# Performance work log

Hardware: AMD Instinct MI355X
Metric: run time of the kernel (lower is better)

## Reference

```python
import jax, jax.numpy as jnp
import numpy as np

DIM = 512
HEADS = 8
DIM_HEAD = 64
HIDDEN = HEADS * DIM_HEAD
SCALE = DIM_HEAD ** -0.5


def rmsnorm_ch(x, g):
    # F.normalize over channel dim (axis=1), then * g * sqrt(C)
    # x: [b, c, l], g: [c]
    n = jnp.maximum(jnp.linalg.norm(x, axis=1, keepdims=True), 1e-12)
    c = x.shape[1]
    return (x / n) * g[None, :, None] * (c ** 0.5)


def setup_inputs() -> dict:
    key = jax.random.key(0)
    ks = jax.random.split(key, 6)
    b, l = 8, 4096
    x = jax.random.normal(ks[0], (b, DIM, l), dtype=jnp.float32)
    g_in = jnp.ones((DIM,), dtype=jnp.float32)
    # conv1d kernel_size=1 == matmul; kaiming-ish init scale
    w_qkv = jax.random.normal(ks[1], (3 * HIDDEN, DIM), dtype=jnp.float32) * (1.0 / np.sqrt(DIM))
    w_out = jax.random.normal(ks[2], (DIM, HIDDEN), dtype=jnp.float32) * (1.0 / np.sqrt(HIDDEN))
    b_out = jax.random.normal(ks[3], (DIM,), dtype=jnp.float32) * 0.01
    g_out = jnp.ones((DIM,), dtype=jnp.float32)
    return {"x": x, "g_in": g_in, "w_qkv": w_qkv, "w_out": w_out, "b_out": b_out, "g_out": g_out}


def reference(x, g_in, w_qkv, w_out, b_out, g_out):
    b, c, l = x.shape
    residual = x
    xn = rmsnorm_ch(x, g_in)                       # [b, c, l]
    qkv = jnp.einsum('oc,bcl->bol', w_qkv, xn)     # [b, 3*hidden, l]
    q, k, v = jnp.split(qkv, 3, axis=1)            # each [b, hidden, l]
    def to_heads(t):
        return t.reshape(b, HEADS, DIM_HEAD, l)    # [b, h, d, l]
    q, k, v = to_heads(q), to_heads(k), to_heads(v)
    q = jax.nn.softmax(q, axis=2) * SCALE          # softmax over head-dim d
    k = jax.nn.softmax(k, axis=3)                  # softmax over sequence l
    context = jnp.einsum('bhdn,bhen->bhde', k, v)  # [b, h, d, e]
    out = jnp.einsum('bhde,bhdn->bhen', context, q)  # [b, h, e, l]
    out = out.reshape(b, HIDDEN, l)
    o = jnp.einsum('ch,bhl->bcl', w_out, out) + b_out[None, :, None]
    o = rmsnorm_ch(o, g_out)
    return o + residual
```

## Files before the change

kernel.cpp:

```cpp
#include <hip/hip_runtime.h>


#define BB 8
#define CC 512
#define LL 4096
#define HH 8
#define DH 64
#define TC 1536

__device__ __constant__ const float SQRT_C = 22.62741699796952f;
#define SCALE_Q 0.125f

typedef unsigned short bfr_t;
typedef __attribute__((ext_vector_type(8))) short short8;
typedef __attribute__((ext_vector_type(4))) float f32x4;

__device__ __forceinline__ float bf2f(bfr_t v) {
  union { unsigned u; float f; } c; c.u = ((unsigned)v) << 16; return c.f;
}
__device__ __forceinline__ bfr_t f2bf(float f) {
  union { float f; unsigned u; } c; c.f = f;
  unsigned u = c.u + 0x7fffu + ((c.u >> 16) & 1u);
  return (bfr_t)(u >> 16);
}

__device__ __forceinline__ void load_lds16(const bfr_t* g, short* l) {
  __builtin_amdgcn_global_load_lds(
      (const __attribute__((address_space(1))) void*)g,
      (__attribute__((address_space(3))) void*)l, 16, 0, 0);
}

__global__ __launch_bounds__(256) void conv_bf16_2(
    const float* __restrict__ in1, bfr_t* __restrict__ o1, int n1,
    const float* __restrict__ in2, bfr_t* __restrict__ o2, int n2) {
  int i8 = (blockIdx.x * 256 + threadIdx.x) * 8;
  const float* src;
  bfr_t* dst;
  if (i8 < n1) { src = in1 + i8; dst = o1 + i8; }
  else {
    int j8 = i8 - n1;
    if (j8 >= n2) return;
    src = in2 + j8; dst = o2 + j8;
  }
  f32x4 a = *(const f32x4*)src;
  f32x4 b = *(const f32x4*)(src + 4);
  union { short s[8]; f32x4 v; } pk;
#pragma unroll
  for (int u = 0; u < 4; ++u) { pk.s[u] = (short)f2bf(a[u]); pk.s[u + 4] = (short)f2bf(b[u]); }
  *(f32x4*)dst = pk.v;
}

__global__ __launch_bounds__(256) void fused_norm_transpose(
    const float* __restrict__ x, const float* __restrict__ g,
    bfr_t* __restrict__ xt) {
  __shared__ float tile[64][65];
  __shared__ float red[4][64];
  __shared__ float invn_s[64];
  int b = blockIdx.y, l0 = blockIdx.x * 64;
  int t = threadIdx.x, ll = t & 63, cg = t >> 6;
  const float* xb = x + (size_t)b * CC * LL + l0;
  float vals[8][16];
  float ss = 0.f;
#pragma unroll
  for (int ch = 0; ch < 8; ++ch) {
    int c0 = ch * 64;
#pragma unroll
    for (int i = 0; i < 16; ++i) {
      int c = i * 4 + cg;
      float v = xb[(size_t)(c0 + c) * LL + ll];
      vals[ch][i] = v;
      ss += v * v;
    }
  }
  red[cg][ll] = ss;
  __syncthreads();
  if (cg == 0) {
    float s = red[0][ll] + red[1][ll] + red[2][ll] + red[3][ll];
    invn_s[ll] = SQRT_C / fmaxf(sqrtf(s), 1e-12f);
  }
  __syncthreads();
  int lw = t >> 2, ccw = (t & 3) * 16;
  float iv = invn_s[lw];
#pragma unroll
  for (int ch = 0; ch < 8; ++ch) {
    int c0 = ch * 64;
#pragma unroll
    for (int i = 0; i < 16; ++i) tile[i * 4 + cg][ll] = vals[ch][i];
    __syncthreads();
    union { short s[16]; f32x4 v[2]; } pk;
#pragma unroll
    for (int u = 0; u < 16; ++u) {
      int c = ccw + u;
      pk.s[u] = (short)f2bf(tile[c][lw] * g[c0 + c] * iv);
    }
    bfr_t* dst = xt + ((size_t)b * LL + l0 + lw) * CC + c0 + ccw;
    *(f32x4*)dst = pk.v[0];
    *(f32x4*)(dst + 8) = pk.v[1];
    __syncthreads();
  }
}

#define NT 8

__device__ __forceinline__ void stage_half(const bfr_t* g, short* l, int wid) {
  load_lds16(g + (size_t)wid * 8192,        l + wid * 1024);
  load_lds16(g + (size_t)wid * 8192 + 4096, l + wid * 1024 + 512);
}

#define CFENCE asm volatile("" ::: "memory")
#define LGKM0 asm volatile("s_waitcnt lgkmcnt(0)" ::: "memory")
#define VMC0  asm volatile("s_waitcnt vmcnt(0)" ::: "memory")
#define SB    __builtin_amdgcn_sched_barrier(0)
#define BAR   do { CFENCE; __builtin_amdgcn_s_barrier(); CFENCE; } while (0)
#define PRIO1 __builtin_amdgcn_s_setprio(1)
#define PRIO0 __builtin_amdgcn_s_setprio(0)

#define DSR(dst, addr, LIT) \
  asm volatile("ds_read_b128 %0, %1 offset:" #LIT : "=v"(dst) : "v"(addr))

#define RD_A(S, L0, L1, L2, L3) do {           \
    DSR(S[0], aAs0, L0); DSR(S[1], aAs1, L0);  \
    DSR(S[2], aAs0, L1); DSR(S[3], aAs1, L1);  \
    DSR(S[4], aAs0, L2); DSR(S[5], aAs1, L2);  \
    DSR(S[6], aAs0, L3); DSR(S[7], aAs1, L3); } while (0)
#define RD_B(S, L0, L1) do {                   \
    DSR(S[0], bBs0, L0); DSR(S[1], bBs1, L0);  \
    DSR(S[2], bBs0, L1); DSR(S[3], bBs1, L1); } while (0)

#define MMA8(QM, QN, AS, BS) do {                                            \
    _Pragma("unroll") for (int i_ = 0; i_ < 4; ++i_)                         \
      _Pragma("unroll") for (int j_ = 0; j_ < 2; ++j_) {                     \
        acc[(QM)*4+i_][(QN)*2+j_] = __builtin_amdgcn_mfma_f32_16x16x32_bf16( \
            AS[i_*2+0], BS[j_*2+0], acc[(QM)*4+i_][(QN)*2+j_], 0, 0, 0);     \
        acc[(QM)*4+i_][(QN)*2+j_] = __builtin_amdgcn_mfma_f32_16x16x32_bf16( \
            AS[i_*2+1], BS[j_*2+1], acc[(QM)*4+i_][(QN)*2+j_], 0, 0, 0);     \
      }                                                                      \
  } while (0)

#define STAGE_T(J, D) do {                                                   \
    stage_half(pA0 + (J) * 64, As + (D) * 16384, wid);                       \
    stage_half(pA1 + (J) * 64, As + (D) * 16384 + 8192, wid);                \
    stage_half(pB0 + (J) * 64, Bs + (D) * 16384, wid);                       \
    stage_half(pB1 + (J) * 64, Bs + (D) * 16384 + 8192, wid);                \
  } while (0)

#define TILE_E(KT) do {                                                      \
                                      \
    PRIO1; RD_B(bS1, 4096, 6144); MMA8(0, 0, aS0, bS0); PRIO0; LGKM0; SB;    \
                                      \
    PRIO1; RD_A(aS1, 8192, 10240, 12288, 14336); MMA8(0, 1, aS0, bS1);       \
    PRIO0; LGKM0; SB;                                                        \
         \
    if ((KT) < 7) { VMC0; }                                                  \
    BAR;                                                                     \
    if ((KT) <= 5) STAGE_T((KT) + 2, 0);                                     \
    PRIO1;                                                                   \
    if ((KT) < 7) RD_A(aS0, 32768, 34816, 36864, 38912);                     \
    MMA8(1, 1, aS1, bS1); PRIO0; LGKM0; SB;                                  \
            \
    PRIO1; MMA8(1, 0, aS1, bS0); PRIO0;                                      \
    if ((KT) < 7) RD_B(bS0, 32768, 34816);                                   \
    LGKM0; SB;                                                               \
  } while (0)

#define TILE_O(KT) do {                                                      \
    PRIO1; RD_B(bS1, 36864, 38912); MMA8(0, 0, aS0, bS0); PRIO0; LGKM0; SB;  \
    PRIO1; RD_A(aS1, 40960, 43008, 45056, 47104); MMA8(0, 1, aS0, bS1);      \
    PRIO0; LGKM0; SB;                                                        \
    if ((KT) < 7) { VMC0; }                                                  \
    BAR;                                                                     \
    if ((KT) <= 5) STAGE_T((KT) + 2, 1);                                     \
    PRIO1;                                                                   \
    if ((KT) < 7) RD_A(aS0, 0, 2048, 4096, 6144);                            \
    MMA8(1, 1, aS1, bS1); PRIO0; LGKM0; SB;                                  \
    PRIO1; MMA8(1, 0, aS1, bS0); PRIO0;                                      \
    if ((KT) < 7) RD_B(bS0, 0, 2048);                                        \
    LGKM0; SB;                                                               \
  } while (0)

__global__ __launch_bounds__(512, 2) void gemm256(
    const bfr_t* __restrict__ A, const bfr_t* __restrict__ Bt,
    bfr_t* __restrict__ Cout, const float* __restrict__ bias, int M) {
  __shared__ short lds[65536];
  short* As = lds;
  short* Bs = lds + 32768;

  int nwg = gridDim.x;
  int gy = M >> 8;
  int bid = blockIdx.x;
  int logical = (bid & 7) * (nwg >> 3) + (bid >> 3);
  int perz = (LL / 256) * gy;
  int bz = logical / perz;
  int rem = logical - bz * perz;
  int bx = rem / gy;
  int by = rem - bx * gy;

  int m0 = by * 256, n0 = bx * 256;
  int t = threadIdx.x, lane = t & 63, wid = t >> 6;
  int quad = lane >> 4, r16 = lane & 15;
  int wm = wid >> 2, wn = wid & 3;
  int soff = (lane >> 3) * 512 + (((lane & 7) ^ (lane >> 3)) * 8);
  int slot0 = (quad ^ (lane & 7)) * 8;
  int slot1 = ((4 + quad) ^ (lane & 7)) * 8;

  unsigned lb = (unsigned)(uintptr_t)(__attribute__((address_space(3))) short*)lds;
  unsigned aAs0 = lb + (unsigned)(wm * 16384 + r16 * 128 + slot0 * 2);
  unsigned aAs1 = lb + (unsigned)(wm * 16384 + r16 * 128 + slot1 * 2);
  unsigned bbase = 65536u + (unsigned)((wn >> 1) * 16384 + ((wn & 1) * 64 + r16) * 128);
  unsigned bBs0 = lb + bbase + (unsigned)(slot0 * 2);
  unsigned bBs1 = lb + bbase + (unsigned)(slot1 * 2);

  const bfr_t* pA0 = A + (size_t)m0 * 512 + soff;
  const bfr_t* pA1 = pA0 + (size_t)128 * 512;
  const bfr_t* pB0 = Bt + (size_t)bz * LL * 512 + (size_t)n0 * 512 + soff;
  const bfr_t* pB1 = pB0 + (size_t)128 * 512;

  f32x4 acc[8][4] = {};
  short8 aS0[8], aS1[8];
  short8 bS0[4], bS1[4];

  STAGE_T(0, 0);
  STAGE_T(1, 1);
  asm volatile("s_waitcnt vmcnt(8)" ::: "memory");
  BAR;
  RD_A(aS0, 0, 2048, 4096, 6144);
  RD_B(bS0, 0, 2048);
  LGKM0; SB;

  TILE_E(0); TILE_O(1); TILE_E(2); TILE_O(3);
  TILE_E(4); TILE_O(5); TILE_E(6); TILE_O(7);

  bfr_t* Cb = Cout + (size_t)bz * M * LL;
  int crow = m0 + wm * 128 + quad * 4;
  int ccol = n0 + wn * 64 + r16;
#pragma unroll
  for (int am = 0; am < 8; ++am) {
    int rbase = crow + (am >> 2) * 64 + (am & 3) * 16;
#pragma unroll
    for (int reg = 0; reg < 4; ++reg) {
      int row = rbase + reg;
      float bi = bias ? bias[row] : 0.f;
#pragma unroll
      for (int an = 0; an < 4; ++an) {
        int col = ccol + (an >> 1) * 32 + (an & 1) * 16;
        Cb[(size_t)row * LL + col] = f2bf(acc[am][an][reg] + bi);
      }
    }
  }
}

__global__ __launch_bounds__(256) void context_mfma(
    const bfr_t* __restrict__ qkv, float* __restrict__ ctx_p,
    float* __restrict__ ksum_p) {
  __shared__ float red[4][4096];
  int s = blockIdx.x, bh = blockIdx.y;
  int b = bh >> 3, h = bh & 7;
  int t = threadIdx.x, lane = t & 63, wid = t >> 6;
  int quad = lane >> 4, r = lane & 15;
  const bfr_t* kb = qkv + ((size_t)b * TC + 512 + h * 64) * LL;
  const bfr_t* vb = qkv + ((size_t)b * TC + 1024 + h * 64) * LL;
  int n_base = s * 512 + wid * 128;
  f32x4 acc[4][4] = {};
  float ps[4] = {};
#pragma unroll
  for (int ks = 0; ks < 4; ++ks) {
    int n0 = n_base + ks * 32;
    short8 af[4], bf8[4];
#pragma unroll
    for (int i = 0; i < 4; ++i) {
      union { short s[8]; short8 v8; } uk;
      uk.v8 = *(const short8*)&kb[(size_t)(i * 16 + r) * LL + n0 + quad * 8];
#pragma unroll
      for (int jj = 0; jj < 8; ++jj) {
        float e = __expf(bf2f((bfr_t)uk.s[jj]));
        uk.s[jj] = (short)f2bf(e);
        ps[i] += e;
      }
      af[i] = uk.v8;
      bf8[i] = *(const short8*)&vb[(size_t)(i * 16 + r) * LL + n0 + quad * 8];
    }
#pragma unroll
    for (int i = 0; i < 4; ++i)
#pragma unroll
      for (int j = 0; j < 4; ++j)
        acc[i][j] = __builtin_amdgcn_mfma_f32_16x16x32_bf16(af[i], bf8[j],
                                                            acc[i][j], 0, 0, 0);
  }
#pragma unroll
  for (int i = 0; i < 4; ++i) {
    ps[i] += __shfl_xor(ps[i], 16, 64);
    ps[i] += __shfl_xor(ps[i], 32, 64);
  }
  if (quad == 0) {
#pragma unroll
    for (int i = 0; i < 4; ++i) red[wid][i * 16 + r] = ps[i];
  }
  __syncthreads();
  if (t < 64)
    ksum_p[((size_t)bh * 8 + s) * 64 + t] =
        red[0][t] + red[1][t] + red[2][t] + red[3][t];
  __syncthreads();
#pragma unroll
  for (int i = 0; i < 4; ++i)
#pragma unroll
    for (int j = 0; j < 4; ++j)
#pragma unroll
      for (int reg = 0; reg < 4; ++reg)
        red[wid][(i * 16 + quad * 4 + reg) * 64 + j * 16 + r] = acc[i][j][reg];
  __syncthreads();
  float* out = ctx_p + ((size_t)bh * 8 + s) * 4096;
#pragma unroll
  for (int u = 0; u < 16; ++u) {
    int idx = u * 256 + t;
    out[idx] = red[0][idx] + red[1][idx] + red[2][idx] + red[3][idx];
  }
}

__global__ __launch_bounds__(256) void context_reduce(
    const float* __restrict__ ctx_p, const float* __restrict__ ksum_p,
    bfr_t* __restrict__ ctx_bf) {
  __shared__ float zinv[64];
  int bh = blockIdx.x;
  int t = threadIdx.x;
  if (t < 64) {
    float s = 0.f;
#pragma unroll
    for (int s8 = 0; s8 < 8; ++s8) s += ksum_p[((size_t)bh * 8 + s8) * 64 + t];
    zinv[t] = 1.f / s;
  }
  __syncthreads();
#pragma unroll
  for (int i = 0; i < 16; ++i) {
    int idx = i * 256 + t;
    int d = idx >> 6;
    float sum = 0.f;
#pragma unroll
    for (int s = 0; s < 8; ++s) sum += ctx_p[((size_t)bh * 8 + s) * 4096 + idx];
    ctx_bf[(size_t)bh * 4096 + idx] = f2bf(sum * zinv[d]);
  }
}

__global__ __launch_bounds__(256) void apply_fused(
    const bfr_t* __restrict__ qkv, const bfr_t* __restrict__ ctx_bf,
    bfr_t* __restrict__ out_t) {
  int b = blockIdx.z, h = blockIdx.y;
  int t = threadIdx.x, lane = t & 63, wid = t >> 6;
  int quad = lane >> 4, r = lane & 15;
  int n0 = blockIdx.x * 256 + wid * 64;
  const bfr_t* qb = qkv + ((size_t)b * TC + h * 64) * LL;
  const bfr_t* cb = ctx_bf + (size_t)(b * HH + h) * 4096;
  float v[4][16];
  float pm[4];
#pragma unroll
  for (int i = 0; i < 4; ++i) {
    pm[i] = -1e30f;
#pragma unroll
    for (int ks = 0; ks < 2; ++ks)
#pragma unroll
      for (int jj = 0; jj < 8; ++jj) {
        float q = bf2f(qb[(size_t)(ks * 32 + quad * 8 + jj) * LL + n0 + i * 16 + r]);
        v[i][ks * 8 + jj] = q;
        pm[i] = fmaxf(pm[i], q);
      }
  }
#pragma unroll
  for (int i = 0; i < 4; ++i) {
    pm[i] = fmaxf(pm[i], __shfl_xor(pm[i], 16, 64));
    pm[i] = fmaxf(pm[i], __shfl_xor(pm[i], 32, 64));
  }
  float psum[4];
#pragma unroll
  for (int i = 0; i < 4; ++i) {
    float s = 0.f;
#pragma unroll
    for (int u = 0; u < 16; ++u) { v[i][u] = __expf(v[i][u] - pm[i]); s += v[i][u]; }
    psum[i] = s;
  }
#pragma unroll
  for (int i = 0; i < 4; ++i) {
    psum[i] += __shfl_xor(psum[i], 16, 64);
    psum[i] += __shfl_xor(psum[i], 32, 64);
  }
  short8 af[2][4];
#pragma unroll
  for (int i = 0; i < 4; ++i) {
    float sc = SCALE_Q / psum[i];
#pragma unroll
    for (int ks = 0; ks < 2; ++ks) {
      union { short s[8]; short8 v8; } u;
#pragma unroll
      for (int jj = 0; jj < 8; ++jj) u.s[jj] = (short)f2bf(v[i][ks * 8 + jj] * sc);
      af[ks][i] = u.v8;
    }
  }
  short8 bfrag[2][4];
#pragma unroll
  for (int ks = 0; ks < 2; ++ks)
#pragma unroll
    for (int j = 0; j < 4; ++j) {
      union { short s[8]; short8 v8; } u;
#pragma unroll
      for (int jj = 0; jj < 8; ++jj)
        u.s[jj] = (short)cb[(ks * 32 + quad * 8 + jj) * 64 + j * 16 + r];
      bfrag[ks][j] = u.v8;
    }
  f32x4 acc[4][4] = {};
#pragma unroll
  for (int ks = 0; ks < 2; ++ks)
#pragma unroll
    for (int i = 0; i < 4; ++i)
#pragma unroll
      for (int j = 0; j < 4; ++j)
        acc[i][j] = __builtin_amdgcn_mfma_f32_16x16x32_bf16(af[ks][i], bfrag[ks][j],
                                                            acc[i][j], 0, 0, 0);
  bfr_t* dst = out_t + (size_t)b * LL * 512 + h * 64;
#pragma unroll
  for (int i = 0; i < 4; ++i)
#pragma unroll
    for (int reg = 0; reg < 4; ++reg) {
      int row = n0 + i * 16 + quad * 4 + reg;
#pragma unroll
      for (int j = 0; j < 4; ++j)
        dst[(size_t)row * 512 + j * 16 + r] = f2bf(acc[i][j][reg]);
    }
}

__global__ __launch_bounds__(256) void final_norm_res(
    const bfr_t* __restrict__ o, const float* __restrict__ g,
    const float* __restrict__ x, float* __restrict__ out) {
  __shared__ float red[4][64];
  __shared__ float invn[64];
  int b = blockIdx.y, l0 = blockIdx.x * 64;
  int t = threadIdx.x, ll = t & 63, cg = t >> 6;
  const bfr_t* ob = o + (size_t)b * CC * LL + l0 + ll;
  unsigned pk[64];
  float ss = 0.f;
#pragma unroll
  for (int i = 0; i < 64; ++i) {
    int c = cg * 128 + 2 * i;
    unsigned u0 = ob[(size_t)c * LL];
    unsigned u1 = ob[(size_t)(c + 1) * LL];
    float v0 = bf2f((bfr_t)u0), v1 = bf2f((bfr_t)u1);
    ss += v0 * v0 + v1 * v1;
    pk[i] = u0 | (u1 << 16);
  }
  red[cg][ll] = ss;
  __syncthreads();
  if (cg == 0) {
    float s = red[0][ll] + red[1][ll] + red[2][ll] + red[3][ll];
    invn[ll] = SQRT_C / fmaxf(sqrtf(s), 1e-12f);
  }
  __syncthreads();
  float iv = invn[ll];
  const float* xb = x + (size_t)b * CC * LL + l0 + ll;
  float* outb = out + (size_t)b * CC * LL + l0 + ll;
#pragma unroll
  for (int i = 0; i < 64; ++i) {
    int c = cg * 128 + 2 * i;
    float v0 = bf2f((bfr_t)(pk[i] & 0xffffu));
    float v1 = bf2f((bfr_t)(pk[i] >> 16));
    outb[(size_t)c * LL] = v0 * g[c] * iv + xb[(size_t)c * LL];
    outb[(size_t)(c + 1) * LL] = v1 * g[c + 1] * iv + xb[(size_t)(c + 1) * LL];
  }
}

extern "C" void kernel_launch(void* const* d_in, const int* in_sizes, int n_in,
                              void* d_out, int out_size, void* d_ws,
                              size_t ws_size, hipStream_t stream) {
  const float* x     = (const float*)d_in[0];
  const float* g_in  = (const float*)d_in[1];
  const float* w_qkv = (const float*)d_in[2];
  const float* w_out = (const float*)d_in[3];
  const float* b_out = (const float*)d_in[4];
  const float* g_out = (const float*)d_in[5];
  float* out = (float*)d_out;

  char* ws = (char*)d_ws;
  const size_t off_wqkv  = 0;
  const size_t off_wout  = 1572864;
  const size_t off_ksump = 2097152;
  const size_t off_ctx   = 2260992;
  const size_t off_ctxp  = 3309568;
  const size_t off_xt    = 11698176;
  const size_t off_qkv   = 45252608;
  const size_t ws_need   = 145915904;
  if (ws_size < ws_need) return;

  bfr_t* wqkv_bf = (bfr_t*)(ws + off_wqkv);
  bfr_t* wout_bf = (bfr_t*)(ws + off_wout);
  float* ksum_p  = (float*)(ws + off_ksump);
  bfr_t* ctx_bf  = (bfr_t*)(ws + off_ctx);
  float* ctxp    = (float*)(ws + off_ctxp);
  bfr_t* xt      = (bfr_t*)(ws + off_xt);
  bfr_t* qkv     = (bfr_t*)(ws + off_qkv);
  bfr_t* o_bf    = (bfr_t*)(ws + off_qkv);

  conv_bf16_2<<<dim3((1536 * 512 + 512 * 512) / 8 / 256), 256, 0, stream>>>(
      w_qkv, wqkv_bf, 1536 * 512, w_out, wout_bf, 512 * 512);
  fused_norm_transpose<<<dim3(LL / 64, BB), 256, 0, stream>>>(x, g_in, xt);
  gemm256<<<dim3((LL / 256) * (TC / 256) * BB), 512, 0, stream>>>(wqkv_bf, xt, qkv, nullptr, TC);
  context_mfma<<<dim3(8, BB * HH), 256, 0, stream>>>(qkv, ctxp, ksum_p);
  context_reduce<<<dim3(BB * HH), 256, 0, stream>>>(ctxp, ksum_p, ctx_bf);
  apply_fused<<<dim3(LL / 256, HH, BB), 256, 0, stream>>>(qkv, ctx_bf, xt);
  gemm256<<<dim3((LL / 256) * (CC / 256) * BB), 512, 0, stream>>>(wout_bf, xt, o_bf, b_out, CC);
  final_norm_res<<<dim3(LL / 64, BB), 256, 0, stream>>>(o_bf, g_out, x, out);
}
```

Measured before the change: 280.9 us.

## Load GEMM A operand directly to registers, stage only B through LDS

The 256x256 GEMM stops staging the weight (A) tile through LDS and instead loads each wave's A fragments straight from global memory into registers, prefetching the next k-step while computing the current one. Only B is double-buffered in LDS, which halves LDS use, and the tile schedule is simplified to a single TILE macro with partial vmcnt waits. Each wave now owns a contiguous 64-column slice of B, so the epilogue column mapping changes. This removes the A-side LDS writes and reads, but adds global-load latency and register pressure, and A data is fetched redundantly by the waves that share the same rows.

```diff
diff --git a/kernel.cpp b/kernel.cpp
--- a/kernel.cpp
+++ b/kernel.cpp
@@ -102,14 +102,9 @@
 
 #define NT 8
 
-__device__ __forceinline__ void stage_half(const bfr_t* g, short* l, int wid) {
-  load_lds16(g + (size_t)wid * 8192,        l + wid * 1024);
-  load_lds16(g + (size_t)wid * 8192 + 4096, l + wid * 1024 + 512);
-}
-
 #define CFENCE asm volatile("" ::: "memory")
 #define LGKM0 asm volatile("s_waitcnt lgkmcnt(0)" ::: "memory")
-#define VMC0  asm volatile("s_waitcnt vmcnt(0)" ::: "memory")
+#define VMCW(N) asm volatile("s_waitcnt vmcnt(" #N ")" ::: "memory")
 #define SB    __builtin_amdgcn_sched_barrier(0)
 #define BAR   do { CFENCE; __builtin_amdgcn_s_barrier(); CFENCE; } while (0)
 #define PRIO1 __builtin_amdgcn_s_setprio(1)
@@ -118,72 +113,58 @@
 #define DSR(dst, addr, LIT) \
   asm volatile("ds_read_b128 %0, %1 offset:" #LIT : "=v"(dst) : "v"(addr))
 
-#define RD_A(S, L0, L1, L2, L3) do {           \
-    DSR(S[0], aAs0, L0); DSR(S[1], aAs1, L0);  \
-    DSR(S[2], aAs0, L1); DSR(S[3], aAs1, L1);  \
-    DSR(S[4], aAs0, L2); DSR(S[5], aAs1, L2);  \
-    DSR(S[6], aAs0, L3); DSR(S[7], aAs1, L3); } while (0)
-#define RD_B(S, L0, L1) do {                   \
-    DSR(S[0], bBs0, L0); DSR(S[1], bBs1, L0);  \
-    DSR(S[2], bBs0, L1); DSR(S[3], bBs1, L1); } while (0)
-
-#define MMA8(QM, QN, AS, BS) do {                                            \
+#define RD_BS0() do {                                      \
+    DSR(bS[0], bA0, 0);    DSR(bS[1], bA1, 0);             \
+    DSR(bS[2], bA0, 2048); DSR(bS[3], bA1, 2048);          \
+    DSR(bS[4], bA0, 4096); DSR(bS[5], bA1, 4096);          \
+    DSR(bS[6], bA0, 6144); DSR(bS[7], bA1, 6144); } while (0)
+#define RD_BS1() do {                                      \
+    DSR(bS[0], bA0, 32768); DSR(bS[1], bA1, 32768);        \
+    DSR(bS[2], bA0, 34816); DSR(bS[3], bA1, 34816);        \
+    DSR(bS[4], bA0, 36864); DSR(bS[5], bA1, 36864);        \
+    DSR(bS[6], bA0, 38912); DSR(bS[7], bA1, 38912); } while (0)
+
+#define LD_A(S, H, J) do {                                                   \
+    _Pragma("unroll") for (int i_ = 0; i_ < 4; ++i_) {                       \
+      S[i_ * 2 + 0] = *(const short8*)(pA + (size_t)((H) * 64 + i_ * 16) * 512 + (J) * 64);      \
+      S[i_ * 2 + 1] = *(const short8*)(pA + (size_t)((H) * 64 + i_ * 16) * 512 + (J) * 64 + 32); \
+    } } while (0)
+
+#define MMA_H(QM, AS) do {                                                   \
+    PRIO1;                                                                   \
     _Pragma("unroll") for (int i_ = 0; i_ < 4; ++i_)                         \
-      _Pragma("unroll") for (int j_ = 0; j_ < 2; ++j_) {                     \
-        acc[(QM)*4+i_][(QN)*2+j_] = __builtin_amdgcn_mfma_f32_16x16x32_bf16( \
-            AS[i_*2+0], BS[j_*2+0], acc[(QM)*4+i_][(QN)*2+j_], 0, 0, 0);     \
-        acc[(QM)*4+i_][(QN)*2+j_] = __builtin_amdgcn_mfma_f32_16x16x32_bf16( \
-            AS[i_*2+1], BS[j_*2+1], acc[(QM)*4+i_][(QN)*2+j_], 0, 0, 0);     \
+      _Pragma("unroll") for (int j_ = 0; j_ < 4; ++j_) {                     \
+        acc[(QM)*4+i_][j_] = __builtin_amdgcn_mfma_f32_16x16x32_bf16(        \
+            AS[i_*2+0], bS[j_*2+0], acc[(QM)*4+i_][j_], 0, 0, 0);            \
+        acc[(QM)*4+i_][j_] = __builtin_amdgcn_mfma_f32_16x16x32_bf16(        \
+            AS[i_*2+1], bS[j_*2+1], acc[(QM)*4+i_][j_], 0, 0, 0);            \
       }                                                                      \
+    PRIO0; } while (0)
+
+#define STAGE_B(J, D) do {                                                   \
+    _Pragma("unroll") for (int u_ = 0; u_ < 4; ++u_)                         \
+      load_lds16(pB + (size_t)(J) * 64 + (size_t)(wid * 4 + u_) * 4096,      \
+                 Bls + (D) * 16384 + (wid * 4 + u_) * 512);                  \
   } while (0)
 
-#define STAGE_T(J, D) do {                                                   \
-    stage_half(pA0 + (J) * 64, As + (D) * 16384, wid);                       \
-    stage_half(pA1 + (J) * 64, As + (D) * 16384 + 8192, wid);                \
-    stage_half(pB0 + (J) * 64, Bs + (D) * 16384, wid);                       \
-    stage_half(pB1 + (J) * 64, Bs + (D) * 16384 + 8192, wid);                \
-  } while (0)
-
-#define TILE_E(KT) do {                                                      \
-                                      \
-    PRIO1; RD_B(bS1, 4096, 6144); MMA8(0, 0, aS0, bS0); PRIO0; LGKM0; SB;    \
-                                      \
-    PRIO1; RD_A(aS1, 8192, 10240, 12288, 14336); MMA8(0, 1, aS0, bS1);       \
-    PRIO0; LGKM0; SB;                                                        \
-         \
-    if ((KT) < 7) { VMC0; }                                                  \
-    BAR;                                                                     \
-    if ((KT) <= 5) STAGE_T((KT) + 2, 0);                                     \
-    PRIO1;                                                                   \
-    if ((KT) < 7) RD_A(aS0, 32768, 34816, 36864, 38912);                     \
-    MMA8(1, 1, aS1, bS1); PRIO0; LGKM0; SB;                                  \
-            \
-    PRIO1; MMA8(1, 0, aS1, bS0); PRIO0;                                      \
-    if ((KT) < 7) RD_B(bS0, 32768, 34816);                                   \
-    LGKM0; SB;                                                               \
-  } while (0)
-
-#define TILE_O(KT) do {                                                      \
-    PRIO1; RD_B(bS1, 36864, 38912); MMA8(0, 0, aS0, bS0); PRIO0; LGKM0; SB;  \
-    PRIO1; RD_A(aS1, 40960, 43008, 45056, 47104); MMA8(0, 1, aS0, bS1);      \
-    PRIO0; LGKM0; SB;                                                        \
-    if ((KT) < 7) { VMC0; }                                                  \
-    BAR;                                                                     \
-    if ((KT) <= 5) STAGE_T((KT) + 2, 1);                                     \
-    PRIO1;                                                                   \
-    if ((KT) < 7) RD_A(aS0, 0, 2048, 4096, 6144);                            \
-    MMA8(1, 1, aS1, bS1); PRIO0; LGKM0; SB;                                  \
-    PRIO1; MMA8(1, 0, aS1, bS0); PRIO0;                                      \
-    if ((KT) < 7) RD_B(bS0, 0, 2048);                                        \
-    LGKM0; SB;                                                               \
+#define TILE(KT, RD) do {                                                    \
+    RD(); LGKM0; SB; BAR;                                                    \
+    MMA_H(0, aS0); SB;                                                       \
+    if ((KT) < NT - 1) LD_A(aS0, 0, (KT) + 1);                               \
+    SB;                                                                      \
+    MMA_H(1, aS1); SB;                                                       \
+    if ((KT) < NT - 1) LD_A(aS1, 1, (KT) + 1);                               \
+    if ((KT) < NT - 2) STAGE_B((KT) + 2, (KT) & 1);                          \
+    SB;                                                                      \
+    if ((KT) == NT - 2)     { VMCW(16); BAR; }                               \
+    else if ((KT) < NT - 2) { VMCW(20); BAR; }                               \
   } while (0)
 
 __global__ __launch_bounds__(512, 2) void gemm256(
     const bfr_t* __restrict__ A, const bfr_t* __restrict__ Bt,
     bfr_t* __restrict__ Cout, const float* __restrict__ bias, int M) {
-  __shared__ short lds[65536];
-  short* As = lds;
-  short* Bs = lds + 32768;
+  __shared__ short lds[32768];
+  short* Bls = lds;
 
   int nwg = gridDim.x;
   int gy = M >> 8;
@@ -200,35 +181,29 @@
   int quad = lane >> 4, r16 = lane & 15;
   int wm = wid >> 2, wn = wid & 3;
   int soff = (lane >> 3) * 512 + (((lane & 7) ^ (lane >> 3)) * 8);
-  int slot0 = (quad ^ (lane & 7)) * 8;
-  int slot1 = ((4 + quad) ^ (lane & 7)) * 8;
+  int slot0 = (quad ^ (lane & 7));
+  int slot1 = ((4 + quad) ^ (lane & 7));
 
   unsigned lb = (unsigned)(uintptr_t)(__attribute__((address_space(3))) short*)lds;
-  unsigned aAs0 = lb + (unsigned)(wm * 16384 + r16 * 128 + slot0 * 2);
-  unsigned aAs1 = lb + (unsigned)(wm * 16384 + r16 * 128 + slot1 * 2);
-  unsigned bbase = 65536u + (unsigned)((wn >> 1) * 16384 + ((wn & 1) * 64 + r16) * 128);
-  unsigned bBs0 = lb + bbase + (unsigned)(slot0 * 2);
-  unsigned bBs1 = lb + bbase + (unsigned)(slot1 * 2);
-
-  const bfr_t* pA0 = A + (size_t)m0 * 512 + soff;
-  const bfr_t* pA1 = pA0 + (size_t)128 * 512;
-  const bfr_t* pB0 = Bt + (size_t)bz * LL * 512 + (size_t)n0 * 512 + soff;
-  const bfr_t* pB1 = pB0 + (size_t)128 * 512;
+  unsigned bA0 = lb + (unsigned)((wn * 64 + r16) * 128 + slot0 * 16);
+  unsigned bA1 = lb + (unsigned)((wn * 64 + r16) * 128 + slot1 * 16);
+
+  const bfr_t* pB = Bt + (size_t)bz * LL * 512 + (size_t)n0 * 512 + soff;
+  const bfr_t* pA = A + (size_t)(m0 + wm * 128 + r16) * 512 + quad * 8;
 
   f32x4 acc[8][4] = {};
   short8 aS0[8], aS1[8];
-  short8 bS0[4], bS1[4];
-
-  STAGE_T(0, 0);
-  STAGE_T(1, 1);
-  asm volatile("s_waitcnt vmcnt(8)" ::: "memory");
+  short8 bS[8];
+
+  STAGE_B(0, 0);
+  STAGE_B(1, 1);
+  LD_A(aS0, 0, 0);
+  LD_A(aS1, 1, 0);
+  VMCW(20);
   BAR;
-  RD_A(aS0, 0, 2048, 4096, 6144);
-  RD_B(bS0, 0, 2048);
-  LGKM0; SB;
-
-  TILE_E(0); TILE_O(1); TILE_E(2); TILE_O(3);
-  TILE_E(4); TILE_O(5); TILE_E(6); TILE_O(7);
+
+  TILE(0, RD_BS0); TILE(1, RD_BS1); TILE(2, RD_BS0); TILE(3, RD_BS1);
+  TILE(4, RD_BS0); TILE(5, RD_BS1); TILE(6, RD_BS0); TILE(7, RD_BS1);
 
   bfr_t* Cb = Cout + (size_t)bz * M * LL;
   int crow = m0 + wm * 128 + quad * 4;
@@ -242,7 +217,7 @@
       float bi = bias ? bias[row] : 0.f;
 #pragma unroll
       for (int an = 0; an < 4; ++an) {
-        int col = ccol + (an >> 1) * 32 + (an & 1) * 16;
+        int col = ccol + an * 16;
         Cb[(size_t)row * LL + col] = f2bf(acc[am][an][reg] + bi);
       }
     }
```

After: 354.8 us. 1.26x slower.
